# Kernel optimization log

Hardware: AMD Instinct MI355X
Metric: run time of the kernel (lower is better)

The kernel has to match this reference:

```python
import jax, jax.numpy as jnp
import numpy as np

N = 262144          # total instances (patches)
E = 512             # encoding_size
H = 256             # attention_hidden_size
NUM_BAGS = 512      # number of bags (slides); max(batch_indices)+1


def setup_inputs() -> dict:
    key = jax.random.key(0)
    k1, k2, k3, k4, k5 = jax.random.split(key, 5)
    bag_encoding = jax.random.normal(k1, (N, E), dtype=jnp.float32)
    idx = jnp.sort(jax.random.randint(k2, (N,), 0, NUM_BAGS))
    # ensure num_bags = max+1 == NUM_BAGS deterministically
    batch_indices = idx.at[0].set(0).at[-1].set(NUM_BAGS - 1)
    # kaiming-uniform-ish fan_in init scales
    Vw = jax.random.uniform(k3, (H, E), jnp.float32, -1.0, 1.0) * np.sqrt(6.0 / E)
    Vb = jnp.zeros((H,), jnp.float32)
    ww = jax.random.uniform(k4, (1, H), jnp.float32, -1.0, 1.0) * np.sqrt(6.0 / H)
    wb = jnp.zeros((1,), jnp.float32)
    dw = jax.random.uniform(k5, (2, E), jnp.float32, -1.0, 1.0) * np.sqrt(6.0 / E)
    db = jnp.zeros((2,), jnp.float32)
    return {"bag_encoding": bag_encoding, "Vw": Vw, "Vb": Vb, "ww": ww,
            "wb": wb, "dw": dw, "db": db, "batch_indices": batch_indices}


def reference(bag_encoding, Vw, Vb, ww, wb, dw, db, batch_indices):
    # attention scores: tanh(V x) -> w -> exp   [N, 1]
    v = jnp.tanh(jnp.einsum('ne,he->nh', bag_encoding, Vw) + Vb)
    alphas = jnp.exp(jnp.einsum('nh,oh->no', v, ww) + wb)  # [N, 1]
    # segment softmax denominator per bag
    sum_alphas = jax.ops.segment_sum(alphas, batch_indices, num_segments=NUM_BAGS)  # [B, 1]
    alphas = alphas / sum_alphas[batch_indices]
    # attention-weighted bag pooling
    bag_sum = jax.ops.segment_sum(alphas * bag_encoding, batch_indices, num_segments=NUM_BAGS)  # [B, E]
    logits = jnp.einsum('be,ce->bc', bag_sum, dw) + db  # [B, 2]
    return jax.nn.softmax(logits, axis=1)
```

## Files before the change

### kernel.cpp

```cpp
#include <hip/hip_runtime.h>
#include <hip/hip_bf16.h>

#define N_INST 262144
#define E_DIM  512
#define H_DIM  256
#define NBAGS  512
#define MI     32
#define XS_STRIDE 520

typedef __bf16 bf16x8 __attribute__((ext_vector_type(8)));
typedef float  f32x4  __attribute__((ext_vector_type(4)));

__global__ void vw_to_bf16(const float* __restrict__ src,
                           __hip_bfloat16* __restrict__ dst) {
    int i = (blockIdx.x * 256 + threadIdx.x) * 4;
    float4 f = *(const float4*)(src + i);
    dst[i + 0] = __float2bfloat16(f.x);
    dst[i + 1] = __float2bfloat16(f.y);
    dst[i + 2] = __float2bfloat16(f.z);
    dst[i + 3] = __float2bfloat16(f.w);
}

__global__ __launch_bounds__(256, 4) void attn_main(
    const float* __restrict__ X,
    const __hip_bfloat16* __restrict__ Vw,
    const float* __restrict__ Vb,
    const float* __restrict__ ww,
    const float* __restrict__ wb,
    const int* __restrict__ bidx,
    float* __restrict__ bag_acc,
    float* __restrict__ sum_alphas)
{
    __shared__ __hip_bfloat16 xs[MI][XS_STRIDE];
    __shared__ float s_part[4][MI];
    __shared__ float a_sh[MI];
    __shared__ int   bag_sh[MI];

    const int tid = threadIdx.x;
    const int i0  = blockIdx.x * MI;

    if (tid < MI) bag_sh[tid] = bidx[i0 + tid];

    {
        const int c4 = tid & 127;
        const int r2 = tid >> 7;
        for (int rr = 0; rr < MI; rr += 2) {
            const int r = rr + r2;
            float4 f = *(const float4*)(X + (size_t)(i0 + r) * E_DIM + c4 * 4);
            __hip_bfloat16* dst = &xs[r][c4 * 4];
            dst[0] = __float2bfloat16(f.x);
            dst[1] = __float2bfloat16(f.y);
            dst[2] = __float2bfloat16(f.z);
            dst[3] = __float2bfloat16(f.w);
        }
    }
    __syncthreads();

    const int wave = tid >> 6;
    const int lane = tid & 63;
    const int l16  = lane & 15;
    const int kgrp = lane >> 4;

    f32x4 acc[2][4];
    for (int mt = 0; mt < 2; mt++)
        for (int nt = 0; nt < 4; nt++)
            acc[mt][nt] = (f32x4){0.f, 0.f, 0.f, 0.f};

    for (int k0 = 0; k0 < E_DIM; k0 += 32) {
        bf16x8 a_frag[2], b_frag[4];
        const int kc = k0 + kgrp * 8;
        for (int nt = 0; nt < 4; nt++) {
            const int h = wave * 64 + nt * 16 + l16;
            b_frag[nt] = *(const bf16x8*)((const __bf16*)Vw + (size_t)h * E_DIM + kc);
        }
        for (int mt = 0; mt < 2; mt++)
            a_frag[mt] = *(const bf16x8*)&xs[mt * 16 + l16][kc];
        for (int mt = 0; mt < 2; mt++)
            for (int nt = 0; nt < 4; nt++)
                acc[mt][nt] = __builtin_amdgcn_mfma_f32_16x16x32_bf16(
                    a_frag[mt], b_frag[nt], acc[mt][nt], 0, 0, 0);
    }

    float ww_r[4], vb_r[4];
    for (int nt = 0; nt < 4; nt++) {
        const int h = wave * 64 + nt * 16 + l16;
        ww_r[nt] = ww[h];
        vb_r[nt] = Vb[h];
    }
    for (int mt = 0; mt < 2; mt++) {
        for (int r = 0; r < 4; r++) {
            float t = 0.f;
            for (int nt = 0; nt < 4; nt++) {
                float v = tanhf(acc[mt][nt][r] + vb_r[nt]);
                t += ww_r[nt] * v;
            }
            for (int off = 1; off < 16; off <<= 1)
                t += __shfl_xor(t, off, 64);
            if (l16 == 0)
                s_part[wave][mt * 16 + kgrp * 4 + r] = t;
        }
    }
    __syncthreads();

    if (tid < MI) {
        float s = s_part[0][tid] + s_part[1][tid] + s_part[2][tid] +
                  s_part[3][tid] + wb[0];
        a_sh[tid] = expf(s);
    }
    __syncthreads();

    {
        const int e0 = tid * 2;
        float c0 = 0.f, c1 = 0.f, asum = 0.f;
        for (int i = 0; i < MI; i++) {
            const float a = a_sh[i];
            __hip_bfloat162 p = *(const __hip_bfloat162*)&xs[i][e0];
            c0 += a * __low2float(p);
            c1 += a * __high2float(p);
            asum += a;
            const bool flush = (i == MI - 1) || (bag_sh[i + 1] != bag_sh[i]);
            if (flush) {
                const int b = bag_sh[i];
                atomicAdd(&bag_acc[(size_t)b * E_DIM + e0], c0);
                atomicAdd(&bag_acc[(size_t)b * E_DIM + e0 + 1], c1);
                if (tid == 0) atomicAdd(&sum_alphas[b], asum);
                c0 = 0.f; c1 = 0.f; asum = 0.f;
            }
        }
    }
}

__global__ void finalize(const float* __restrict__ bag_acc,
                         const float* __restrict__ sum_alphas,
                         const float* __restrict__ dw,
                         const float* __restrict__ db,
                         float* __restrict__ out) {
    const int b = blockIdx.x;
    const int lane = threadIdx.x;
    const float sa = sum_alphas[b];
    const float inv = (sa > 0.f) ? (1.f / sa) : 0.f;
    float l0 = 0.f, l1 = 0.f;
    for (int e = lane; e < E_DIM; e += 64) {
        const float bs = bag_acc[(size_t)b * E_DIM + e] * inv;
        l0 += bs * dw[e];
        l1 += bs * dw[E_DIM + e];
    }
    for (int off = 32; off; off >>= 1) {
        l0 += __shfl_xor(l0, off, 64);
        l1 += __shfl_xor(l1, off, 64);
    }
    if (lane == 0) {
        l0 += db[0];
        l1 += db[1];
        const float m  = fmaxf(l0, l1);
        const float e0 = expf(l0 - m), e1 = expf(l1 - m);
        const float is = 1.f / (e0 + e1);
        out[b * 2 + 0] = e0 * is;
        out[b * 2 + 1] = e1 * is;
    }
}

extern "C" void kernel_launch(void* const* d_in, const int* in_sizes, int n_in,
                              void* d_out, int out_size, void* d_ws, size_t ws_size,
                              hipStream_t stream) {
    const float* X   = (const float*)d_in[0];
    const float* Vwf = (const float*)d_in[1];
    const float* Vb  = (const float*)d_in[2];
    const float* ww  = (const float*)d_in[3];
    const float* wb  = (const float*)d_in[4];
    const float* dw  = (const float*)d_in[5];
    const float* db  = (const float*)d_in[6];
    const int*  bidx = (const int*)d_in[7];
    float* out = (float*)d_out;

    __hip_bfloat16* Vwb = (__hip_bfloat16*)d_ws;
    float* bag_acc    = (float*)((char*)d_ws + (size_t)H_DIM * E_DIM * 2);
    float* sum_alphas = bag_acc + (size_t)NBAGS * E_DIM;

    hipMemsetAsync(bag_acc, 0, ((size_t)NBAGS * E_DIM + NBAGS) * sizeof(float), stream);
    vw_to_bf16<<<H_DIM * E_DIM / 1024, 256, 0, stream>>>(Vwf, Vwb);
    attn_main<<<N_INST / MI, 256, 0, stream>>>(X, Vwb, Vb, ww, wb, bidx,
                                               bag_acc, sum_alphas);
    finalize<<<NBAGS, 64, 0, stream>>>(bag_acc, sum_alphas, dw, db, out);
}
```

Baseline: 860.1 us.

## Convert attention kernel to persistent blocks with register-resident weights and double buffering

Replaces the one-tile-per-block launch with 256 persistent 512-thread blocks, each processing 32 consecutive tiles. Vw fragments are loaded once into registers, the next X tile is prefetched into a second LDS buffer while MFMAs run on the current one, and bag partial sums are carried across tiles so fewer atomics are issued. It also swaps tanhf/expf for exp+rcp approximations. The cost is heavy register pressure from the 32 resident B fragments, and only 256 blocks on the device, which may limit occupancy and latency hiding.

```diff
diff --git a/kernel.cpp b/kernel.cpp
--- a/kernel.cpp
+++ b/kernel.cpp
@@ -7,9 +7,16 @@
 #define NBAGS  512
 #define MI     32
 #define XS_STRIDE 520
+#define NBLOCKS 256
+#define TILES_PER_BLK (N_INST / MI / NBLOCKS)
 
 typedef __bf16 bf16x8 __attribute__((ext_vector_type(8)));
 typedef float  f32x4  __attribute__((ext_vector_type(4)));
+
+__device__ __forceinline__ float fast_tanh(float x) {
+    float e = __expf(2.0f * x);
+    return 1.0f - 2.0f * __builtin_amdgcn_rcpf(e + 1.0f);
+}
 
 __global__ void vw_to_bf16(const float* __restrict__ src,
                            __hip_bfloat16* __restrict__ dst) {
@@ -21,7 +28,7 @@
     dst[i + 3] = __float2bfloat16(f.w);
 }
 
-__global__ __launch_bounds__(256, 4) void attn_main(
+__global__ __launch_bounds__(512, 2) void attn_persist(
     const float* __restrict__ X,
     const __hip_bfloat16* __restrict__ Vw,
     const float* __restrict__ Vb,
@@ -31,102 +38,149 @@
     float* __restrict__ bag_acc,
     float* __restrict__ sum_alphas)
 {
-    __shared__ __hip_bfloat16 xs[MI][XS_STRIDE];
-    __shared__ float s_part[4][MI];
+    __shared__ __hip_bfloat16 xs[2][MI][XS_STRIDE];
+    __shared__ float s_part[8][MI];
     __shared__ float a_sh[MI];
-    __shared__ int   bag_sh[MI];
-
-    const int tid = threadIdx.x;
-    const int i0  = blockIdx.x * MI;
-
-    if (tid < MI) bag_sh[tid] = bidx[i0 + tid];
-
+    __shared__ int   bag_sh[2][MI];
+
+    const int tid  = threadIdx.x;
+    const int wave = tid >> 6;
+    const int lane = tid & 63;
+    const int l16  = lane & 15;
+    const int kgrp = lane >> 4;
+
+    const int tile0 = blockIdx.x * TILES_PER_BLK;
+
+    bf16x8 breg[16][2];
+    float ww_r[2], vb_r[2];
     {
-        const int c4 = tid & 127;
-        const int r2 = tid >> 7;
-        for (int rr = 0; rr < MI; rr += 2) {
-            const int r = rr + r2;
-            float4 f = *(const float4*)(X + (size_t)(i0 + r) * E_DIM + c4 * 4);
-            __hip_bfloat16* dst = &xs[r][c4 * 4];
+        const __bf16* Vwp = (const __bf16*)Vw;
+        #pragma unroll
+        for (int nt = 0; nt < 2; nt++) {
+            const int h = wave * 32 + nt * 16 + l16;
+            ww_r[nt] = ww[h];
+            vb_r[nt] = Vb[h];
+            #pragma unroll
+            for (int k = 0; k < 16; k++)
+                breg[k][nt] = *(const bf16x8*)(Vwp + (size_t)h * E_DIM + k * 32 + kgrp * 8);
+        }
+    }
+
+    const int c4 = tid & 127;
+    const int r0 = tid >> 7;
+
+    {
+        const size_t i0 = (size_t)tile0 * MI;
+        #pragma unroll
+        for (int rr = 0; rr < 8; rr++) {
+            const int r = rr * 4 + r0;
+            float4 f = *(const float4*)(X + (i0 + r) * E_DIM + c4 * 4);
+            __hip_bfloat16* dst = &xs[0][r][c4 * 4];
             dst[0] = __float2bfloat16(f.x);
             dst[1] = __float2bfloat16(f.y);
             dst[2] = __float2bfloat16(f.z);
             dst[3] = __float2bfloat16(f.w);
         }
+        if (tid < MI) bag_sh[0][tid] = bidx[i0 + tid];
     }
     __syncthreads();
 
-    const int wave = tid >> 6;
-    const int lane = tid & 63;
-    const int l16  = lane & 15;
-    const int kgrp = lane >> 4;
-
-    f32x4 acc[2][4];
-    for (int mt = 0; mt < 2; mt++)
-        for (int nt = 0; nt < 4; nt++)
-            acc[mt][nt] = (f32x4){0.f, 0.f, 0.f, 0.f};
-
-    for (int k0 = 0; k0 < E_DIM; k0 += 32) {
-        bf16x8 a_frag[2], b_frag[4];
-        const int kc = k0 + kgrp * 8;
-        for (int nt = 0; nt < 4; nt++) {
-            const int h = wave * 64 + nt * 16 + l16;
-            b_frag[nt] = *(const bf16x8*)((const __bf16*)Vw + (size_t)h * E_DIM + kc);
-        }
+    int   cur_bag = -1;
+    float col_acc = 0.f;
+    float asum    = 0.f;
+
+    int p = 0;
+    for (int it = 0; it < TILES_PER_BLK; it++) {
+        const size_t inst0 = (size_t)(tile0 + it) * MI;
+        const bool has_next = (it + 1 < TILES_PER_BLK);
+
+        float4 ld[8];
+        if (has_next) {
+            const size_t i1 = inst0 + MI;
+            #pragma unroll
+            for (int rr = 0; rr < 8; rr++)
+                ld[rr] = *(const float4*)(X + (i1 + rr * 4 + r0) * E_DIM + c4 * 4);
+        }
+
+        f32x4 acc[2][2];
+        #pragma unroll
         for (int mt = 0; mt < 2; mt++)
-            a_frag[mt] = *(const bf16x8*)&xs[mt * 16 + l16][kc];
-        for (int mt = 0; mt < 2; mt++)
-            for (int nt = 0; nt < 4; nt++)
-                acc[mt][nt] = __builtin_amdgcn_mfma_f32_16x16x32_bf16(
-                    a_frag[mt], b_frag[nt], acc[mt][nt], 0, 0, 0);
-    }
-
-    float ww_r[4], vb_r[4];
-    for (int nt = 0; nt < 4; nt++) {
-        const int h = wave * 64 + nt * 16 + l16;
-        ww_r[nt] = ww[h];
-        vb_r[nt] = Vb[h];
-    }
-    for (int mt = 0; mt < 2; mt++) {
-        for (int r = 0; r < 4; r++) {
-            float t = 0.f;
-            for (int nt = 0; nt < 4; nt++) {
-                float v = tanhf(acc[mt][nt][r] + vb_r[nt]);
-                t += ww_r[nt] * v;
+            #pragma unroll
+            for (int nt = 0; nt < 2; nt++)
+                acc[mt][nt] = (f32x4){0.f, 0.f, 0.f, 0.f};
+
+        #pragma unroll
+        for (int k = 0; k < 16; k++) {
+            bf16x8 a_frag[2];
+            #pragma unroll
+            for (int mt = 0; mt < 2; mt++)
+                a_frag[mt] = *(const bf16x8*)&xs[p][mt * 16 + l16][k * 32 + kgrp * 8];
+            #pragma unroll
+            for (int mt = 0; mt < 2; mt++)
+                #pragma unroll
+                for (int nt = 0; nt < 2; nt++)
+                    acc[mt][nt] = __builtin_amdgcn_mfma_f32_16x16x32_bf16(
+                        a_frag[mt], breg[k][nt], acc[mt][nt], 0, 0, 0);
+        }
+
+        if (has_next) {
+            #pragma unroll
+            for (int rr = 0; rr < 8; rr++) {
+                const int r = rr * 4 + r0;
+                __hip_bfloat16* dst = &xs[p ^ 1][r][c4 * 4];
+                dst[0] = __float2bfloat16(ld[rr].x);
+                dst[1] = __float2bfloat16(ld[rr].y);
+                dst[2] = __float2bfloat16(ld[rr].z);
+                dst[3] = __float2bfloat16(ld[rr].w);
             }
-            for (int off = 1; off < 16; off <<= 1)
-                t += __shfl_xor(t, off, 64);
-            if (l16 == 0)
-                s_part[wave][mt * 16 + kgrp * 4 + r] = t;
-        }
-    }
-    __syncthreads();
-
-    if (tid < MI) {
-        float s = s_part[0][tid] + s_part[1][tid] + s_part[2][tid] +
-                  s_part[3][tid] + wb[0];
-        a_sh[tid] = expf(s);
-    }
-    __syncthreads();
-
-    {
-        const int e0 = tid * 2;
-        float c0 = 0.f, c1 = 0.f, asum = 0.f;
+            if (tid < MI) bag_sh[p ^ 1][tid] = bidx[inst0 + MI + tid];
+        }
+
+        #pragma unroll
+        for (int mt = 0; mt < 2; mt++) {
+            #pragma unroll
+            for (int r = 0; r < 4; r++) {
+                float t = 0.f;
+                #pragma unroll
+                for (int nt = 0; nt < 2; nt++)
+                    t += ww_r[nt] * fast_tanh(acc[mt][nt][r] + vb_r[nt]);
+                #pragma unroll
+                for (int off = 1; off < 16; off <<= 1)
+                    t += __shfl_xor(t, off, 64);
+                if (l16 == 0)
+                    s_part[wave][mt * 16 + kgrp * 4 + r] = t;
+            }
+        }
+        __syncthreads();
+
+        if (tid < MI) {
+            float s = wb[0];
+            #pragma unroll
+            for (int w = 0; w < 8; w++) s += s_part[w][tid];
+            a_sh[tid] = __expf(s);
+        }
+        __syncthreads();
+
         for (int i = 0; i < MI; i++) {
+            const int b = bag_sh[p][i];
+            if (b != cur_bag) {
+                if (cur_bag >= 0) {
+                    atomicAdd(&bag_acc[(size_t)cur_bag * E_DIM + tid], col_acc);
+                    if (tid == 0) atomicAdd(&sum_alphas[cur_bag], asum);
+                }
+                cur_bag = b; col_acc = 0.f; asum = 0.f;
+            }
             const float a = a_sh[i];
-            __hip_bfloat162 p = *(const __hip_bfloat162*)&xs[i][e0];
-            c0 += a * __low2float(p);
-            c1 += a * __high2float(p);
-            asum += a;
-            const bool flush = (i == MI - 1) || (bag_sh[i + 1] != bag_sh[i]);
-            if (flush) {
-                const int b = bag_sh[i];
-                atomicAdd(&bag_acc[(size_t)b * E_DIM + e0], c0);
-                atomicAdd(&bag_acc[(size_t)b * E_DIM + e0 + 1], c1);
-                if (tid == 0) atomicAdd(&sum_alphas[b], asum);
-                c0 = 0.f; c1 = 0.f; asum = 0.f;
-            }
-        }
+            col_acc += a * __bfloat162float(xs[p][i][tid]);
+            asum    += a;
+        }
+        __syncthreads();
+        p ^= 1;
+    }
+
+    if (cur_bag >= 0) {
+        atomicAdd(&bag_acc[(size_t)cur_bag * E_DIM + tid], col_acc);
+        if (tid == 0) atomicAdd(&sum_alphas[cur_bag], asum);
     }
 }
 
@@ -179,7 +233,7 @@
 
     hipMemsetAsync(bag_acc, 0, ((size_t)NBAGS * E_DIM + NBAGS) * sizeof(float), stream);
     vw_to_bf16<<<H_DIM * E_DIM / 1024, 256, 0, stream>>>(Vwf, Vwb);
-    attn_main<<<N_INST / MI, 256, 0, stream>>>(X, Vwb, Vb, ww, wb, bidx,
-                                               bag_acc, sum_alphas);
+    attn_persist<<<NBLOCKS, 512, 0, stream>>>(X, Vwb, Vb, ww, wb, bidx,
+                                              bag_acc, sum_alphas);
     finalize<<<NBAGS, 64, 0, stream>>>(bag_acc, sum_alphas, dw, db, out);
 }
```

New measurement: 759.9 us. -11.7%, faster.
